# Kernel tuning notes

Hardware: AMD Instinct MI355X
Metric: run time of the kernel (lower is better)

Reference implementation:

```python
import jax, jax.numpy as jnp
import numpy as np

D_MODEL, D_INNER, D_STATE, D_CONV, DT_RANK = 1024, 2048, 16, 4, 64
BATCH, SEQLEN = 4, 2048


def setup_inputs() -> dict:
    key = jax.random.key(0)
    ks = jax.random.split(key, 10)
    def n(k, shape, scale=1.0):
        return (jax.random.normal(k, shape, dtype=jnp.float32) * scale)
    # A_log = log of positive values in (0, d_state] like the torch init
    A_log = jnp.log(jax.random.uniform(ks[7], (D_INNER, D_STATE), dtype=jnp.float32, minval=0.5, maxval=float(D_STATE)))
    return {
        "hidden_states": n(ks[0], (BATCH, SEQLEN, D_MODEL)),
        "in_proj_w": n(ks[1], (2 * D_INNER, D_MODEL), D_MODEL ** -0.5),
        "conv_w": n(ks[2], (D_INNER, D_CONV), D_CONV ** -0.5),
        "conv_b": n(ks[3], (D_INNER,), 0.1),
        "x_proj_w": n(ks[4], (DT_RANK + 2 * D_STATE, D_INNER), D_INNER ** -0.5),
        "dt_proj_w": n(ks[5], (D_INNER, DT_RANK), DT_RANK ** -0.5),
        "dt_proj_b": n(ks[6], (D_INNER,), 0.5),
        "A_log": A_log,
        "D": jnp.ones((D_INNER,), dtype=jnp.float32),
        "out_proj_w": n(ks[8], (D_MODEL, D_INNER), D_INNER ** -0.5),
    }


def _silu(x):
    return x * jax.nn.sigmoid(x)


def _mamba_forward(hidden_states, in_proj_w, conv_w, conv_b, x_proj_w,
                   dt_proj_w, dt_proj_b, A_log, D, out_proj_w):
    B, L, _ = hidden_states.shape
    d_inner, d_conv = conv_w.shape
    d_state = A_log.shape[1]
    dt_rank = dt_proj_w.shape[1]

    # in_proj (no bias): (b, l, 2*d_inner)
    xz = jnp.einsum('bld,ed->ble', hidden_states, in_proj_w)
    x, z = xz[..., :d_inner], xz[..., d_inner:]

    # causal depthwise conv1d (padding = d_conv-1, truncated to L) + SiLU
    x_pad = jnp.pad(x, ((0, 0), (d_conv - 1, 0), (0, 0)))  # (b, L+d_conv-1, d)
    x_conv = sum(x_pad[:, w:w + L, :] * conv_w[:, w] for w in range(d_conv)) + conv_b
    x_conv = _silu(x_conv)  # (b, l, d_inner)

    # x_proj -> dt, B, C
    x_dbl = jnp.einsum('bld,ed->ble', x_conv, x_proj_w)  # (b, l, dt_rank+2*d_state)
    dt_in = x_dbl[..., :dt_rank]
    Bv = x_dbl[..., dt_rank:dt_rank + d_state]  # (b, l, n)
    Cv = x_dbl[..., dt_rank + d_state:]         # (b, l, n)

    delta = jax.nn.softplus(jnp.einsum('blr,dr->bld', dt_in, dt_proj_w) + dt_proj_b)
    A = -jnp.exp(A_log)  # (d, n), entries negative

    # selective scan over time: state h is (b, d, n)
    def step(h, inp):
        d_t, B_t, C_t, u_t = inp  # (b,d), (b,n), (b,n), (b,d)
        dA = jnp.exp(d_t[:, :, None] * A)                          # (b, d, n)
        h = h * dA + (d_t * u_t)[:, :, None] * B_t[:, None, :]     # (b, d, n)
        y = jnp.einsum('bdn,bn->bd', h, C_t)                       # (b, d)
        return h, y

    h0 = jnp.zeros((B, d_inner, d_state), dtype=hidden_states.dtype)
    xs = (jnp.swapaxes(delta, 0, 1), jnp.swapaxes(Bv, 0, 1),
          jnp.swapaxes(Cv, 0, 1), jnp.swapaxes(x_conv, 0, 1))
    _, ys = jax.lax.scan(step, h0, xs)  # (l, b, d)
    y = jnp.swapaxes(ys, 0, 1) + x_conv * D  # skip term D * u
    y = y * _silu(z)                           # gating

    # out_proj (no bias)
    return jnp.einsum('bld,md->blm', y, out_proj_w)


def reference(hidden_states, in_proj_w, conv_w, conv_b, x_proj_w,
              dt_proj_w, dt_proj_b, A_log, D, out_proj_w):
    return _mamba_forward(hidden_states, in_proj_w, conv_w, conv_b, x_proj_w,
                          dt_proj_w, dt_proj_b, A_log, D, out_proj_w)
```

## Files before the change

kernel.cpp:

```cpp
#include <hip/hip_runtime.h>
#include <hip/hip_bf16.h>

constexpr int BATCH = 4, SEQLEN = 2048, DM = 1024, DI = 2048, DS = 16, DC = 4, DTR = 64;
constexpr int M = BATCH * SEQLEN;
constexpr int NXZ = 2 * DI;
constexpr int NXDBL = DTR + 2 * DS;
constexpr int CL = 64;
constexpr int NCH = SEQLEN / CL;
constexpr size_t CS = (size_t)BATCH * DI * DS;
constexpr float L2E = 1.44269504088896f;

typedef __attribute__((ext_vector_type(8))) short short8;
typedef __attribute__((ext_vector_type(4))) float f32x4;

__device__ __forceinline__ float fexp2(float x) { return __builtin_amdgcn_exp2f(x); }
__device__ __forceinline__ float frcp(float x) { return __builtin_amdgcn_rcpf(x); }
__device__ __forceinline__ float fsig(float z) {
  return frcp(1.f + fexp2(-L2E * z));
}
__device__ __forceinline__ float softplus_fast(float x) {
  return (x > 20.f) ? x
                    : 0.693147180559945f * __builtin_amdgcn_logf(1.f + fexp2(x * L2E));
}

__device__ __forceinline__ void load_lds16(const void* g, void* l) {
  __builtin_amdgcn_global_load_lds(
      (const __attribute__((address_space(1))) unsigned int*)g,
      (__attribute__((address_space(3))) unsigned int*)l, 16, 0, 0);
}

__device__ __forceinline__ void vwaitn(int n) {
  switch (n) {
    case 0: asm volatile("s_waitcnt vmcnt(0)" ::: "memory"); break;
    case 2: asm volatile("s_waitcnt vmcnt(2)" ::: "memory"); break;
    default: asm volatile("s_waitcnt vmcnt(8)" ::: "memory"); break;
  }
}

__global__ __launch_bounds__(256) void k_cvt(const float* __restrict__ s,
                                             __hip_bfloat16* __restrict__ d, int n) {
  int i = (blockIdx.x * 256 + threadIdx.x) * 4;
  if (i + 3 < n) {
    float4 v = *reinterpret_cast<const float4*>(s + i);
    d[i + 0] = __float2bfloat16(v.x);
    d[i + 1] = __float2bfloat16(v.y);
    d[i + 2] = __float2bfloat16(v.z);
    d[i + 3] = __float2bfloat16(v.w);
  }
}

__global__ __launch_bounds__(256) void k_cvt4(const float* __restrict__ p0, int n0, __hip_bfloat16* __restrict__ q0,
                                              const float* __restrict__ p1, int n1, __hip_bfloat16* __restrict__ q1,
                                              const float* __restrict__ p2, int n2, __hip_bfloat16* __restrict__ q2,
                                              const float* __restrict__ p3, int n3, __hip_bfloat16* __restrict__ q3) {
  int i = (blockIdx.x * 256 + threadIdx.x) * 4;
  const float* s;
  __hip_bfloat16* d;
  if (i < n0) { s = p0; d = q0; }
  else if ((i -= n0) < n1) { s = p1; d = q1; }
  else if ((i -= n1) < n2) { s = p2; d = q2; }
  else if ((i -= n2) < n3) { s = p3; d = q3; }
  else return;
  float4 v = *reinterpret_cast<const float4*>(s + i);
  d[i + 0] = __float2bfloat16(v.x);
  d[i + 1] = __float2bfloat16(v.y);
  d[i + 2] = __float2bfloat16(v.z);
  d[i + 3] = __float2bfloat16(v.w);
}

__global__ __launch_bounds__(256) void k_prepA(const float* __restrict__ alog,
                                               float* __restrict__ an, int n) {
  int i = blockIdx.x * 256 + threadIdx.x;
  if (i < n) an[i] = -__expf(alog[i]) * L2E;
}

__global__ __launch_bounds__(256) void k_prepCW(const float* __restrict__ cw,
                                                float* __restrict__ cwt) {
  int i = blockIdx.x * 256 + threadIdx.x;
  if (i < DI * DC) {
    int d = i >> 2, w = i & 3;
    cwt[w * DI + d] = cw[i];
  }
}

template <int OUTMODE>
__global__ __launch_bounds__(512, 2) void k_gemm8(const __hip_bfloat16* __restrict__ A, int lda,
                                                  const __hip_bfloat16* __restrict__ Bm, int ldb,
                                                  void* __restrict__ Cp, int ldc, int K) {
  constexpr int BK = 64;
  const int tid = threadIdx.x;
  const int wid = tid >> 6, l = tid & 63;
  const int wr = wid >> 2, wc = wid & 3;
  const int bm0 = blockIdx.y * 256, bn0 = blockIdx.x * 256;
  const int NT = K / BK;

  __shared__ short LDS[65536];

  const int gc8 = (l & 7) ^ ((l >> 3) & 7);
  const __hip_bfloat16* Abase = A + (size_t)(bm0 + wid * 8 + (l >> 3)) * lda + gc8 * 8;
  const __hip_bfloat16* Bbase = Bm + (size_t)(bn0 + wid * 8 + (l >> 3)) * ldb + gc8 * 8;
  const int wslot = wid * 512;

  const int c8k0 = ((l >> 4) ^ (l & 7)) * 8;
  const int c8k1 = ((4 + (l >> 4)) ^ (l & 7)) * 8;
  const int aoff0 = wr * 8192 + (l & 15) * 64;
  const int boff0 = 32768 + (wc >> 1) * 8192 + (wc & 1) * 4096 + (l & 15) * 64;

  f32x4 acc[8][4] = {};
  short8 a[4][2], b0[2][2], b1[2][2];

  auto stageA = [&](int d, int h, int kt) {
#pragma unroll
    for (int g = 0; g < 2; g++)
      load_lds16(Abase + (size_t)(h * 128 + g * 64) * lda + kt * BK,
                 &LDS[d * 16384 + h * 8192 + g * 4096 + wslot]);
  };
  auto stageB = [&](int d, int h, int kt) {
#pragma unroll
    for (int g = 0; g < 2; g++)
      load_lds16(Bbase + (size_t)(h * 128 + g * 64) * ldb + kt * BK,
                 &LDS[32768 + d * 16384 + h * 8192 + g * 4096 + wslot]);
  };

  stageA(0, 0, 0); stageA(0, 1, 0); stageB(0, 0, 0); stageB(0, 1, 0);

  for (int t = 0; t < NT; t++) {
    const int d = t & 1;
    const int adb = aoff0 + d * 16384;
    const int bdb = boff0 + d * 16384;
    const bool pf = (t + 1 < NT);
    if (pf) stageA(d ^ 1, 0, t + 1);
    vwaitn(pf ? 2 : 0);
    __builtin_amdgcn_sched_barrier(0);
    __builtin_amdgcn_s_barrier();
#pragma unroll
    for (int i = 0; i < 4; i++) {
      a[i][0] = *reinterpret_cast<const short8*>(&LDS[adb + i * 1024 + c8k0]);
      a[i][1] = *reinterpret_cast<const short8*>(&LDS[adb + i * 1024 + c8k1]);
    }
#pragma unroll
    for (int j = 0; j < 2; j++) {
      b0[j][0] = *reinterpret_cast<const short8*>(&LDS[bdb + j * 1024 + c8k0]);
      b0[j][1] = *reinterpret_cast<const short8*>(&LDS[bdb + j * 1024 + c8k1]);
    }
    __builtin_amdgcn_sched_barrier(0);
    __builtin_amdgcn_s_setprio(1);
#pragma unroll
    for (int i = 0; i < 4; i++)
#pragma unroll
      for (int j = 0; j < 2; j++)
#pragma unroll
        for (int ks = 0; ks < 2; ks++)
          acc[i][j] = __builtin_amdgcn_mfma_f32_16x16x32_bf16(a[i][ks], b0[j][ks], acc[i][j], 0, 0, 0);
    __builtin_amdgcn_s_setprio(0);
    __builtin_amdgcn_sched_barrier(0);
    __builtin_amdgcn_s_barrier();
    if (pf) stageA(d ^ 1, 1, t + 1);
#pragma unroll
    for (int j = 0; j < 2; j++) {
      b1[j][0] = *reinterpret_cast<const short8*>(&LDS[bdb + (2 + j) * 1024 + c8k0]);
      b1[j][1] = *reinterpret_cast<const short8*>(&LDS[bdb + (2 + j) * 1024 + c8k1]);
    }
    __builtin_amdgcn_sched_barrier(0);
    __builtin_amdgcn_s_setprio(1);
#pragma unroll
    for (int i = 0; i < 4; i++)
#pragma unroll
      for (int j = 0; j < 2; j++)
#pragma unroll
        for (int ks = 0; ks < 2; ks++)
          acc[i][2 + j] = __builtin_amdgcn_mfma_f32_16x16x32_bf16(a[i][ks], b1[j][ks], acc[i][2 + j], 0, 0, 0);
    __builtin_amdgcn_s_setprio(0);
    __builtin_amdgcn_sched_barrier(0);
    __builtin_amdgcn_s_barrier();
    if (pf) stageB(d ^ 1, 0, t + 1);
#pragma unroll
    for (int i = 0; i < 4; i++) {
      a[i][0] = *reinterpret_cast<const short8*>(&LDS[adb + (4 + i) * 1024 + c8k0]);
      a[i][1] = *reinterpret_cast<const short8*>(&LDS[adb + (4 + i) * 1024 + c8k1]);
    }
    __builtin_amdgcn_sched_barrier(0);
    __builtin_amdgcn_s_setprio(1);
#pragma unroll
    for (int i = 0; i < 4; i++)
#pragma unroll
      for (int j = 0; j < 2; j++)
#pragma unroll
        for (int ks = 0; ks < 2; ks++)
          acc[4 + i][2 + j] = __builtin_amdgcn_mfma_f32_16x16x32_bf16(a[i][ks], b1[j][ks], acc[4 + i][2 + j], 0, 0, 0);
    __builtin_amdgcn_s_setprio(0);
    __builtin_amdgcn_sched_barrier(0);
    __builtin_amdgcn_s_barrier();
    if (pf) stageB(d ^ 1, 1, t + 1);
    __builtin_amdgcn_sched_barrier(0);
    __builtin_amdgcn_s_setprio(1);
#pragma unroll
    for (int i = 0; i < 4; i++)
#pragma unroll
      for (int j = 0; j < 2; j++)
#pragma unroll
        for (int ks = 0; ks < 2; ks++)
          acc[4 + i][j] = __builtin_amdgcn_mfma_f32_16x16x32_bf16(a[i][ks], b0[j][ks], acc[4 + i][j], 0, 0, 0);
    __builtin_amdgcn_s_setprio(0);
    __builtin_amdgcn_sched_barrier(0);
  }

  const int crow0 = bm0 + wr * 128 + (l >> 4) * 4;
  const int ccol0 = bn0 + wc * 64 + (l & 15);
#pragma unroll
  for (int im = 0; im < 8; im++)
#pragma unroll
    for (int jn = 0; jn < 4; jn++) {
      const int col = ccol0 + jn * 16;
#pragma unroll
      for (int r = 0; r < 4; r++) {
        const int row = crow0 + im * 16 + r;
        float v = acc[im][jn][r];
        if constexpr (OUTMODE == 0)
          reinterpret_cast<float*>(Cp)[(size_t)row * ldc + col] = v;
        else
          reinterpret_cast<__hip_bfloat16*>(Cp)[(size_t)row * ldc + col] = __float2bfloat16(v);
      }
    }
}

template <int BM, int BN, int OUTMODE>
__global__ __launch_bounds__(256) void k_gemm_dl(const __hip_bfloat16* __restrict__ A, int lda,
                                                 const __hip_bfloat16* __restrict__ Bm, int ldb,
                                                 void* __restrict__ Cp, int ldc, int K,
                                                 const float* __restrict__ bias) {
  constexpr int BK = 32;
  constexpr int WM = BM / 2, WN = BN / 2;
  constexpr int FM = WM / 16, FN = WN / 16;

  const int tid = threadIdx.x;
  const int wid = tid >> 6, lane = tid & 63;
  const int wm = wid >> 1, wn = wid & 1;
  const int bm0 = blockIdx.y * BM, bn0 = blockIdx.x * BN;
  int kz = 0;
  if constexpr (OUTMODE == 4) kz = blockIdx.z;

  __shared__ short As[BM * BK];
  __shared__ short Bs[BN * BK];

  f32x4 acc[FM][FN] = {};

  const int lrow = lane & 15;
  const int lk = (lane >> 4) * 8;
  const int srow = wid * 16 + (lane >> 2);
  const int scol = (lane & 3) * 8;

  const __hip_bfloat16* Ag = &A[(size_t)(bm0 + srow) * lda + scol + (size_t)kz * K];
  const __hip_bfloat16* Bg = &Bm[(size_t)(bn0 + srow) * ldb + scol + (size_t)kz * K];

  for (int k0 = 0; k0 < K; k0 += BK) {
    __syncthreads();
#pragma unroll
    for (int i = 0; i < (BM + 63) / 64; i++)
      load_lds16(Ag + (size_t)i * 64 * lda + k0, &As[(i * 64 + wid * 16) * BK]);
#pragma unroll
    for (int i = 0; i < (BN + 63) / 64; i++)
      if ((BN % 64 == 0) || (i * 64 + wid * 16 < BN))
        load_lds16(Bg + (size_t)i * 64 * ldb + k0, &Bs[(i * 64 + wid * 16) * BK]);
    __syncthreads();

    short8 af[FM], bf[FN];
#pragma unroll
    for (int i = 0; i < FM; i++)
      af[i] = *reinterpret_cast<const short8*>(&As[(wm * WM + i * 16 + lrow) * BK + lk]);
#pragma unroll
    for (int j = 0; j < FN; j++)
      bf[j] = *reinterpret_cast<const short8*>(&Bs[(wn * WN + j * 16 + lrow) * BK + lk]);
#pragma unroll
    for (int i = 0; i < FM; i++)
#pragma unroll
      for (int j = 0; j < FN; j++)
        acc[i][j] = __builtin_amdgcn_mfma_f32_16x16x32_bf16(af[i], bf[j], acc[i][j], 0, 0, 0);
  }

  const int crow0 = bm0 + wm * WM + (lane >> 4) * 4;
  const int ccol0 = bn0 + wn * WN + lrow;
#pragma unroll
  for (int i = 0; i < FM; i++)
#pragma unroll
    for (int j = 0; j < FN; j++) {
      const int col = ccol0 + j * 16;
      float bv = 0.f;
      if constexpr (OUTMODE == 2) bv = bias[col];
#pragma unroll
      for (int r = 0; r < 4; r++) {
        const int row = crow0 + i * 16 + r;
        float v = acc[i][j][r];
        if constexpr (OUTMODE == 0) {
          reinterpret_cast<float*>(Cp)[(size_t)row * ldc + col] = v;
        } else if constexpr (OUTMODE == 1) {
          reinterpret_cast<__hip_bfloat16*>(Cp)[(size_t)row * ldc + col] = __float2bfloat16(v);
        } else if constexpr (OUTMODE == 2) {
          reinterpret_cast<__hip_bfloat16*>(Cp)[(size_t)row * ldc + col] =
              __float2bfloat16(softplus_fast(v + bv));
        } else {
          reinterpret_cast<float*>(Cp)[(size_t)kz * M * NXDBL + (size_t)row * ldc + col] = v;
        }
      }
    }
}

__global__ __launch_bounds__(256) void k_xred(const float* __restrict__ part,
                                              float* __restrict__ xdbl,
                                              __hip_bfloat16* __restrict__ dtin) {
  int i = (blockIdx.x * 256 + threadIdx.x) * 4;
  float4 s = *reinterpret_cast<const float4*>(part + i);
#pragma unroll
  for (int p = 1; p < 8; p++) {
    const float4 v = *reinterpret_cast<const float4*>(part + (size_t)p * M * NXDBL + i);
    s.x += v.x; s.y += v.y; s.z += v.z; s.w += v.w;
  }
  *reinterpret_cast<float4*>(xdbl + i) = s;
  int c = i % NXDBL;
  if (c < DTR) {
    int m = i / NXDBL;
    __hip_bfloat16* dp = dtin + (size_t)m * DTR + c;
    dp[0] = __float2bfloat16(s.x);
    dp[1] = __float2bfloat16(s.y);
    dp[2] = __float2bfloat16(s.z);
    dp[3] = __float2bfloat16(s.w);
  }
}

__global__ __launch_bounds__(256) void k_conv8(const __hip_bfloat16* __restrict__ xz,
                                               const float* __restrict__ cwt,
                                               const float* __restrict__ cb,
                                               __hip_bfloat16* __restrict__ xc) {
  const int ml = blockIdx.x;
  const int d0 = threadIdx.x * 8;
  const int l = ml & (SEQLEN - 1);
  float acc[8];
  {
    float4 b0 = *reinterpret_cast<const float4*>(cb + d0);
    float4 b1 = *reinterpret_cast<const float4*>(cb + d0 + 4);
    acc[0] = b0.x; acc[1] = b0.y; acc[2] = b0.z; acc[3] = b0.w;
    acc[4] = b1.x; acc[5] = b1.y; acc[6] = b1.z; acc[7] = b1.w;
  }
#pragma unroll
  for (int w = 0; w < DC; w++) {
    int li = l - 3 + w;
    if (li >= 0) {
      short8 xv = *reinterpret_cast<const short8*>(&xz[(size_t)(ml - 3 + w) * NXZ + d0]);
      float4 w0 = *reinterpret_cast<const float4*>(cwt + w * DI + d0);
      float4 w1 = *reinterpret_cast<const float4*>(cwt + w * DI + d0 + 4);
      float wf[8] = {w0.x, w0.y, w0.z, w0.w, w1.x, w1.y, w1.z, w1.w};
#pragma unroll
      for (int j = 0; j < 8; j++) {
        float x = __bfloat162float(__ushort_as_bfloat16((unsigned short)xv[j]));
        acc[j] = fmaf(x, wf[j], acc[j]);
      }
    }
  }
  unsigned short o[8];
#pragma unroll
  for (int j = 0; j < 8; j++)
    o[j] = __bfloat16_as_ushort(__float2bfloat16(acc[j] * fsig(acc[j])));
  *reinterpret_cast<short8*>(&xc[(size_t)ml * DI + d0]) = *reinterpret_cast<short8*>(o);
}

__global__ __launch_bounds__(256) void k_scan1(const __hip_bfloat16* __restrict__ delta_b,
                                               const float* __restrict__ xdbl,
                                               const __hip_bfloat16* __restrict__ xc,
                                               const float* __restrict__ Aneg2,
                                               __hip_bfloat16* __restrict__ Pb,
                                               __hip_bfloat16* __restrict__ Sb) {
  const int tid = threadIdx.x;
  const int d = blockIdx.x * 256 + tid;
  const int c = blockIdx.y, b = blockIdx.z;
  const size_t row0 = (size_t)b * SEQLEN + (size_t)c * CL;

  __shared__ float Bs[CL][16];
  {
    int i = tid * 4;
    int li = i >> 4, n0 = i & 15;
    const float* src = &xdbl[(row0 + li) * NXDBL + DTR + n0];
    *reinterpret_cast<float4*>(&Bs[li][n0]) = *reinterpret_cast<const float4*>(src);
  }

  float Ar[DS];
#pragma unroll
  for (int n = 0; n < DS; n++) Ar[n] = Aneg2[d * DS + n];
  __syncthreads();

  float h[DS] = {};
  float sdelta = 0.f;
  size_t idx = row0 * DI + d;
  float nx_dt = __bfloat162float(delta_b[idx]);
  float nx_u = __bfloat162float(xc[idx]);
  for (int ls = 0; ls < CL; ls++) {
    float delta = nx_dt;
    float u = nx_u;
    if (ls + 1 < CL) {
      size_t idx2 = idx + DI;
      nx_dt = __bfloat162float(delta_b[idx2]);
      nx_u = __bfloat162float(xc[idx2]);
    }
    idx += DI;
    sdelta += delta;
    float du = delta * u;
#pragma unroll
    for (int n = 0; n < DS; n++) {
      float dA = fexp2(delta * Ar[n]);
      h[n] = fmaf(h[n], dA, du * Bs[ls][n]);
    }
  }

  size_t base = (size_t)c * CS + ((size_t)b * DI + d) * DS;
  unsigned short sp[DS], ss[DS];
#pragma unroll
  for (int n = 0; n < DS; n++) {
    ss[n] = __bfloat16_as_ushort(__float2bfloat16(h[n]));
    sp[n] = __bfloat16_as_ushort(__float2bfloat16(fexp2(Ar[n] * sdelta)));
  }
#pragma unroll
  for (int q = 0; q < 2; q++) {
    *reinterpret_cast<short8*>(&Sb[base + q * 8]) = *reinterpret_cast<short8*>(&ss[q * 8]);
    *reinterpret_cast<short8*>(&Pb[base + q * 8]) = *reinterpret_cast<short8*>(&sp[q * 8]);
  }
}

__global__ __launch_bounds__(256) void k_scan2(const __hip_bfloat16* __restrict__ Pb,
                                               const __hip_bfloat16* __restrict__ Sb,
                                               __hip_bfloat16* __restrict__ Hin) {
  size_t t = (size_t)blockIdx.x * 256 + threadIdx.x;
  float h = 0.f;
  for (int c = 0; c < NCH; c++) {
    size_t o = (size_t)c * CS + t;
    Hin[o] = __float2bfloat16(h);
    h = fmaf(__bfloat162float(Pb[o]), h, __bfloat162float(Sb[o]));
  }
}

__global__ __launch_bounds__(256) void k_scan3(const __hip_bfloat16* __restrict__ delta_b,
                                               const float* __restrict__ xdbl,
                                               const __hip_bfloat16* __restrict__ xc,
                                               const __hip_bfloat16* __restrict__ xz,
                                               const float* __restrict__ Aneg2,
                                               const float* __restrict__ Dw,
                                               const __hip_bfloat16* __restrict__ Hin,
                                               __hip_bfloat16* __restrict__ yg) {
  const int tid = threadIdx.x;
  const int d = blockIdx.x * 256 + tid;
  const int c = blockIdx.y, b = blockIdx.z;
  const size_t row0 = (size_t)b * SEQLEN + (size_t)c * CL;

  __shared__ float BCs[CL][32];
  {
    int i = tid * 8;
    int li = i >> 5, n0 = i & 31;
    const float* src = &xdbl[(row0 + li) * NXDBL + DTR + n0];
    *reinterpret_cast<float4*>(&BCs[li][n0]) = *reinterpret_cast<const float4*>(src);
    *reinterpret_cast<float4*>(&BCs[li][n0 + 4]) = *reinterpret_cast<const float4*>(src + 4);
  }

  float Ar[DS];
#pragma unroll
  for (int n = 0; n < DS; n++) Ar[n] = Aneg2[d * DS + n];
  const float Dv = Dw[d];

  float h[DS];
  {
    size_t hbase = (size_t)c * CS + ((size_t)b * DI + d) * DS;
#pragma unroll
    for (int q = 0; q < 2; q++) {
      short8 hv = *reinterpret_cast<const short8*>(&Hin[hbase + q * 8]);
#pragma unroll
      for (int n = 0; n < 8; n++)
        h[q * 8 + n] = __bfloat162float(__ushort_as_bfloat16((unsigned short)hv[n]));
    }
  }
  __syncthreads();

  size_t idx = row0 * DI + d;
  float nx_dt = __bfloat162float(delta_b[idx]);
  float nx_u = __bfloat162float(xc[idx]);
  float nx_z = __bfloat162float(xz[row0 * NXZ + DI + d]);
  for (int ls = 0; ls < CL; ls++) {
    const size_t cur = idx;
    float delta = nx_dt;
    float u = nx_u;
    float zv = nx_z;
    if (ls + 1 < CL) {
      size_t idx2 = idx + DI;
      nx_dt = __bfloat162float(delta_b[idx2]);
      nx_u = __bfloat162float(xc[idx2]);
      nx_z = __bfloat162float(xz[(row0 + ls + 1) * NXZ + DI + d]);
    }
    idx += DI;
    float du = delta * u;
    float y0 = 0.f, y1 = 0.f, y2 = 0.f, y3 = 0.f;
#pragma unroll
    for (int q = 0; q < 4; q++) {
#pragma unroll
      for (int n4 = 0; n4 < 4; n4++) {
        const int n = q * 4 + n4;
        float dA = fexp2(delta * Ar[n]);
        h[n] = fmaf(h[n], dA, du * BCs[ls][n]);
        if (q == 0) y0 = fmaf(h[n], BCs[ls][16 + n], y0);
        else if (q == 1) y1 = fmaf(h[n], BCs[ls][16 + n], y1);
        else if (q == 2) y2 = fmaf(h[n], BCs[ls][16 + n], y2);
        else y3 = fmaf(h[n], BCs[ls][16 + n], y3);
      }
    }
    float y = (y0 + y1) + (y2 + y3);
    float out = (y + u * Dv) * (zv * fsig(zv));
    yg[cur] = __float2bfloat16(out);
  }
}

extern "C" void kernel_launch(void* const* d_in, const int* in_sizes, int n_in,
                              void* d_out, int out_size, void* d_ws, size_t ws_size,
                              hipStream_t stream) {
  const float* hs = (const float*)d_in[0];
  const float* w_in = (const float*)d_in[1];
  const float* conv_w = (const float*)d_in[2];
  const float* conv_b = (const float*)d_in[3];
  const float* w_xp = (const float*)d_in[4];
  const float* w_dt = (const float*)d_in[5];
  const float* dt_b = (const float*)d_in[6];
  const float* A_log = (const float*)d_in[7];
  const float* Dw = (const float*)d_in[8];
  const float* w_out = (const float*)d_in[9];
  float* out = (float*)d_out;

  char* ws = (char*)d_ws;
  size_t off = 0;
  auto alloc = [&](size_t bytes) {
    void* p = ws + off;
    off += (bytes + 255) & ~(size_t)255;
    return p;
  };

  __hip_bfloat16* hs_b   = (__hip_bfloat16*)alloc((size_t)M * DM * 2);
  __hip_bfloat16* win_b  = (__hip_bfloat16*)alloc((size_t)NXZ * DM * 2);
  __hip_bfloat16* wxp_b  = (__hip_bfloat16*)alloc((size_t)NXDBL * DI * 2);
  __hip_bfloat16* wdt_b  = (__hip_bfloat16*)alloc((size_t)DI * DTR * 2);
  __hip_bfloat16* wout_b = (__hip_bfloat16*)alloc((size_t)DM * DI * 2);
  float*          Aneg2  = (float*)alloc((size_t)DI * DS * 4);
  float*          cwt    = (float*)alloc((size_t)DC * DI * 4);
  __hip_bfloat16* xz_b   = (__hip_bfloat16*)alloc((size_t)M * NXZ * 2);
  __hip_bfloat16* xc_b   = (__hip_bfloat16*)alloc((size_t)M * DI * 2);
  float*          xdbl   = (float*)alloc((size_t)M * NXDBL * 4);
  __hip_bfloat16* dtin_b = (__hip_bfloat16*)alloc((size_t)M * DTR * 2);
  __hip_bfloat16* delta_b= (__hip_bfloat16*)alloc((size_t)M * DI * 2);
  __hip_bfloat16* yg_b   = (__hip_bfloat16*)alloc((size_t)M * DI * 2);

  float* xpart = (float*)(ws + 0);
  __hip_bfloat16* Pb  = (__hip_bfloat16*)(ws + 0);
  __hip_bfloat16* Sb  = (__hip_bfloat16*)(ws + ((size_t)8 << 20));
  __hip_bfloat16* Hin = (__hip_bfloat16*)(ws + ((size_t)16 << 20));

  k_cvt<<<(M * DM) / 1024, 256, 0, stream>>>(hs, hs_b, M * DM);
  k_cvt4<<<(NXZ * DM + NXDBL * DI + DI * DTR + DM * DI) / 1024, 256, 0, stream>>>(
      w_in, NXZ * DM, win_b, w_xp, NXDBL * DI, wxp_b, w_dt, DI * DTR, wdt_b,
      w_out, DM * DI, wout_b);
  k_prepA<<<(DI * DS) / 256, 256, 0, stream>>>(A_log, Aneg2, DI * DS);
  k_prepCW<<<(DI * DC + 255) / 256, 256, 0, stream>>>(conv_w, cwt);

  k_gemm8<1><<<dim3(NXZ / 256, M / 256), 512, 0, stream>>>(
      hs_b, DM, win_b, DM, xz_b, NXZ, DM);

  k_conv8<<<M, 256, 0, stream>>>(xz_b, cwt, conv_b, xc_b);

  k_gemm_dl<64, 96, 4><<<dim3(1, M / 64, 8), 256, 0, stream>>>(
      xc_b, DI, wxp_b, DI, xpart, NXDBL, DI / 8, nullptr);
  k_xred<<<(M * NXDBL) / 1024, 256, 0, stream>>>(xpart, xdbl, dtin_b);

  k_gemm_dl<128, 128, 2><<<dim3(DI / 128, M / 128), 256, 0, stream>>>(
      dtin_b, DTR, wdt_b, DTR, delta_b, DI, DTR, dt_b);

  k_scan1<<<dim3(DI / 256, NCH, BATCH), 256, 0, stream>>>(delta_b, xdbl, xc_b,
                                                          Aneg2, Pb, Sb);
  k_scan2<<<(int)(CS / 256), 256, 0, stream>>>(Pb, Sb, Hin);
  k_scan3<<<dim3(DI / 256, NCH, BATCH), 256, 0, stream>>>(delta_b, xdbl, xc_b,
                                                          xz_b, Aneg2, Dw, Hin, yg_b);

  k_gemm_dl<128, 128, 0><<<dim3(DM / 128, M / 128), 256, 0, stream>>>(
      yg_b, DI, wout_b, DI, out, DM, DI, nullptr);
}
```

Before: 322.3 us.

## Use 256x128 triple-buffered GEMM with XCD-aware block remap for in/out projections

Shrinks the in_proj GEMM tile from 256x256 to 256x128 and replaces double buffering with a three-slot LDS ring that prefetches two k-steps ahead. Each iteration now has a single barrier instead of four. Block indices are remapped so consecutive workgroups are spread across the eight XCDs. The out_proj GEMM moves from the generic 128x128 kernel to this new kernel; the output-mode-1 branch is dropped from the generic kernel. The smaller tile doubles the workgroup count for better occupancy and balance, at the cost of more B-matrix reloads per output.

Measured after the change: 312.7 us. -3.0%, faster.

```diff
diff --git a/kernel.cpp b/kernel.cpp
--- a/kernel.cpp
+++ b/kernel.cpp
@@ -33,6 +33,7 @@
   switch (n) {
     case 0: asm volatile("s_waitcnt vmcnt(0)" ::: "memory"); break;
     case 2: asm volatile("s_waitcnt vmcnt(2)" ::: "memory"); break;
+    case 6: asm volatile("s_waitcnt vmcnt(6)" ::: "memory"); break;
     default: asm volatile("s_waitcnt vmcnt(8)" ::: "memory"); break;
   }
 }
@@ -84,17 +85,25 @@
 }
 
 template <int OUTMODE>
-__global__ __launch_bounds__(512, 2) void k_gemm8(const __hip_bfloat16* __restrict__ A, int lda,
-                                                  const __hip_bfloat16* __restrict__ Bm, int ldb,
-                                                  void* __restrict__ Cp, int ldc, int K) {
+__global__ __launch_bounds__(512, 2) void k_gemm8b(const __hip_bfloat16* __restrict__ A, int lda,
+                                                   const __hip_bfloat16* __restrict__ Bm, int ldb,
+                                                   void* __restrict__ Cp, int ldc, int K) {
   constexpr int BK = 64;
+  constexpr int SS = 24576;
   const int tid = threadIdx.x;
   const int wid = tid >> 6, l = tid & 63;
   const int wr = wid >> 2, wc = wid & 3;
-  const int bm0 = blockIdx.y * 256, bn0 = blockIdx.x * 256;
+
+  const int gx = gridDim.x;
+  int nlin = blockIdx.y * gx + blockIdx.x;
+  {
+    const int nwg = gx * gridDim.y;
+    nlin = (nlin & 7) * (nwg >> 3) + (nlin >> 3);
+  }
+  const int bm0 = (nlin / gx) * 256, bn0 = (nlin % gx) * 128;
   const int NT = K / BK;
 
-  __shared__ short LDS[65536];
+  __shared__ short LDS[3 * SS];
 
   const int gc8 = (l & 7) ^ ((l >> 3) & 7);
   const __hip_bfloat16* Abase = A + (size_t)(bm0 + wid * 8 + (l >> 3)) * lda + gc8 * 8;
@@ -104,35 +113,36 @@
   const int c8k0 = ((l >> 4) ^ (l & 7)) * 8;
   const int c8k1 = ((4 + (l >> 4)) ^ (l & 7)) * 8;
   const int aoff0 = wr * 8192 + (l & 15) * 64;
-  const int boff0 = 32768 + (wc >> 1) * 8192 + (wc & 1) * 4096 + (l & 15) * 64;
-
-  f32x4 acc[8][4] = {};
-  short8 a[4][2], b0[2][2], b1[2][2];
-
-  auto stageA = [&](int d, int h, int kt) {
+  const int boff0 = 16384 + (wc * 32 + (l & 15)) * 64;
+
+  f32x4 acc[8][2] = {};
+  short8 a[4][2], b[2][2];
+
+  auto stageA = [&](int slot, int kt) {
+#pragma unroll
+    for (int g = 0; g < 4; g++)
+      load_lds16(Abase + (size_t)(g * 64) * lda + kt * BK,
+                 &LDS[slot * SS + g * 4096 + wslot]);
+  };
+  auto stageB = [&](int slot, int kt) {
 #pragma unroll
     for (int g = 0; g < 2; g++)
-      load_lds16(Abase + (size_t)(h * 128 + g * 64) * lda + kt * BK,
-                 &LDS[d * 16384 + h * 8192 + g * 4096 + wslot]);
+      load_lds16(Bbase + (size_t)(g * 64) * ldb + kt * BK,
+                 &LDS[slot * SS + 16384 + g * 4096 + wslot]);
   };
-  auto stageB = [&](int d, int h, int kt) {
-#pragma unroll
-    for (int g = 0; g < 2; g++)
-      load_lds16(Bbase + (size_t)(h * 128 + g * 64) * ldb + kt * BK,
-                 &LDS[32768 + d * 16384 + h * 8192 + g * 4096 + wslot]);
-  };
-
-  stageA(0, 0, 0); stageA(0, 1, 0); stageB(0, 0, 0); stageB(0, 1, 0);
+
+  stageA(0, 0); stageB(0, 0);
+  stageA(1, 1); stageB(1, 1);
 
   for (int t = 0; t < NT; t++) {
-    const int d = t & 1;
-    const int adb = aoff0 + d * 16384;
-    const int bdb = boff0 + d * 16384;
-    const bool pf = (t + 1 < NT);
-    if (pf) stageA(d ^ 1, 0, t + 1);
-    vwaitn(pf ? 2 : 0);
-    __builtin_amdgcn_sched_barrier(0);
+    const int slot = t % 3;
+    const int sbase = slot * SS;
+    const int s2 = (t + 2) % 3;
+    const bool pf2 = (t + 2 < NT);
+    vwaitn((t + 1 < NT) ? 6 : 0);
     __builtin_amdgcn_s_barrier();
+    const int adb = sbase + aoff0;
+    const int bdb = sbase + boff0;
 #pragma unroll
     for (int i = 0; i < 4; i++) {
       a[i][0] = *reinterpret_cast<const short8*>(&LDS[adb + i * 1024 + c8k0]);
@@ -140,9 +150,10 @@
     }
 #pragma unroll
     for (int j = 0; j < 2; j++) {
-      b0[j][0] = *reinterpret_cast<const short8*>(&LDS[bdb + j * 1024 + c8k0]);
-      b0[j][1] = *reinterpret_cast<const short8*>(&LDS[bdb + j * 1024 + c8k1]);
-    }
+      b[j][0] = *reinterpret_cast<const short8*>(&LDS[bdb + j * 1024 + c8k0]);
+      b[j][1] = *reinterpret_cast<const short8*>(&LDS[bdb + j * 1024 + c8k1]);
+    }
+    if (pf2) stageA(s2, t + 2);
     __builtin_amdgcn_sched_barrier(0);
     __builtin_amdgcn_s_setprio(1);
 #pragma unroll
@@ -151,34 +162,15 @@
       for (int j = 0; j < 2; j++)
 #pragma unroll
         for (int ks = 0; ks < 2; ks++)
-          acc[i][j] = __builtin_amdgcn_mfma_f32_16x16x32_bf16(a[i][ks], b0[j][ks], acc[i][j], 0, 0, 0);
+          acc[i][j] = __builtin_amdgcn_mfma_f32_16x16x32_bf16(a[i][ks], b[j][ks], acc[i][j], 0, 0, 0);
     __builtin_amdgcn_s_setprio(0);
     __builtin_amdgcn_sched_barrier(0);
-    __builtin_amdgcn_s_barrier();
-    if (pf) stageA(d ^ 1, 1, t + 1);
-#pragma unroll
-    for (int j = 0; j < 2; j++) {
-      b1[j][0] = *reinterpret_cast<const short8*>(&LDS[bdb + (2 + j) * 1024 + c8k0]);
-      b1[j][1] = *reinterpret_cast<const short8*>(&LDS[bdb + (2 + j) * 1024 + c8k1]);
-    }
-    __builtin_amdgcn_sched_barrier(0);
-    __builtin_amdgcn_s_setprio(1);
-#pragma unroll
-    for (int i = 0; i < 4; i++)
-#pragma unroll
-      for (int j = 0; j < 2; j++)
-#pragma unroll
-        for (int ks = 0; ks < 2; ks++)
-          acc[i][2 + j] = __builtin_amdgcn_mfma_f32_16x16x32_bf16(a[i][ks], b1[j][ks], acc[i][2 + j], 0, 0, 0);
-    __builtin_amdgcn_s_setprio(0);
-    __builtin_amdgcn_sched_barrier(0);
-    __builtin_amdgcn_s_barrier();
-    if (pf) stageB(d ^ 1, 0, t + 1);
 #pragma unroll
     for (int i = 0; i < 4; i++) {
       a[i][0] = *reinterpret_cast<const short8*>(&LDS[adb + (4 + i) * 1024 + c8k0]);
       a[i][1] = *reinterpret_cast<const short8*>(&LDS[adb + (4 + i) * 1024 + c8k1]);
     }
+    if (pf2) stageB(s2, t + 2);
     __builtin_amdgcn_sched_barrier(0);
     __builtin_amdgcn_s_setprio(1);
 #pragma unroll
@@ -187,30 +179,17 @@
       for (int j = 0; j < 2; j++)
 #pragma unroll
         for (int ks = 0; ks < 2; ks++)
-          acc[4 + i][2 + j] = __builtin_amdgcn_mfma_f32_16x16x32_bf16(a[i][ks], b1[j][ks], acc[4 + i][2 + j], 0, 0, 0);
+          acc[4 + i][j] = __builtin_amdgcn_mfma_f32_16x16x32_bf16(a[i][ks], b[j][ks], acc[4 + i][j], 0, 0, 0);
     __builtin_amdgcn_s_setprio(0);
     __builtin_amdgcn_sched_barrier(0);
-    __builtin_amdgcn_s_barrier();
-    if (pf) stageB(d ^ 1, 1, t + 1);
-    __builtin_amdgcn_sched_barrier(0);
-    __builtin_amdgcn_s_setprio(1);
-#pragma unroll
-    for (int i = 0; i < 4; i++)
-#pragma unroll
-      for (int j = 0; j < 2; j++)
-#pragma unroll
-        for (int ks = 0; ks < 2; ks++)
-          acc[4 + i][j] = __builtin_amdgcn_mfma_f32_16x16x32_bf16(a[i][ks], b0[j][ks], acc[4 + i][j], 0, 0, 0);
-    __builtin_amdgcn_s_setprio(0);
-    __builtin_amdgcn_sched_barrier(0);
   }
 
   const int crow0 = bm0 + wr * 128 + (l >> 4) * 4;
-  const int ccol0 = bn0 + wc * 64 + (l & 15);
+  const int ccol0 = bn0 + wc * 32 + (l & 15);
 #pragma unroll
   for (int im = 0; im < 8; im++)
 #pragma unroll
-    for (int jn = 0; jn < 4; jn++) {
+    for (int jn = 0; jn < 2; jn++) {
       const int col = ccol0 + jn * 16;
 #pragma unroll
       for (int r = 0; r < 4; r++) {
@@ -293,8 +272,6 @@
         float v = acc[i][j][r];
         if constexpr (OUTMODE == 0) {
           reinterpret_cast<float*>(Cp)[(size_t)row * ldc + col] = v;
-        } else if constexpr (OUTMODE == 1) {
-          reinterpret_cast<__hip_bfloat16*>(Cp)[(size_t)row * ldc + col] = __float2bfloat16(v);
         } else if constexpr (OUTMODE == 2) {
           reinterpret_cast<__hip_bfloat16*>(Cp)[(size_t)row * ldc + col] =
               __float2bfloat16(softplus_fast(v + bv));
@@ -562,7 +539,7 @@
   k_prepA<<<(DI * DS) / 256, 256, 0, stream>>>(A_log, Aneg2, DI * DS);
   k_prepCW<<<(DI * DC + 255) / 256, 256, 0, stream>>>(conv_w, cwt);
 
-  k_gemm8<1><<<dim3(NXZ / 256, M / 256), 512, 0, stream>>>(
+  k_gemm8b<1><<<dim3(NXZ / 128, M / 256), 512, 0, stream>>>(
       hs_b, DM, win_b, DM, xz_b, NXZ, DM);
 
   k_conv8<<<M, 256, 0, stream>>>(xz_b, cwt, conv_b, xc_b);
@@ -580,6 +557,6 @@
   k_scan3<<<dim3(DI / 256, NCH, BATCH), 256, 0, stream>>>(delta_b, xdbl, xc_b,
                                                           xz_b, Aneg2, Dw, Hin, yg_b);
 
-  k_gemm_dl<128, 128, 0><<<dim3(DM / 128, M / 128), 256, 0, stream>>>(
-      yg_b, DI, wout_b, DI, out, DM, DI, nullptr);
-}
+  k_gemm8b<0><<<dim3(DM / 128, M / 256), 512, 0, stream>>>(
+      yg_b, DI, wout_b, DI, out, DM, DI);
+}
```
